# Optimization experiments

Hardware: AMD Instinct MI355X
Metric: run time of the kernel (lower is better)

Reference implementation:

```python
import jax, jax.numpy as jnp
import numpy as np

HID = 64      # hidden_dim
HEADS = 4     # attention heads
CH = HID // HEADS  # 16 per-head channels
EDIM = 6      # edge_dim
NEG = 0.2     # leaky_relu negative slope


def _glorot(key, shape):
    fan_in, fan_out = shape[0], shape[-1]
    s = np.sqrt(6.0 / (fan_in + fan_out)).astype(np.float32)
    return jax.random.uniform(key, shape, jnp.float32, -s, s)


def setup_inputs() -> dict:
    key = jax.random.key(0)
    ks = iter(jax.random.split(key, 48))
    N, E, T = 100000, 1200000, 20000
    inp = {
        "x": jax.random.normal(next(ks), (N, 7), jnp.float32),
        "pos": jax.random.normal(next(ks), (N, 3), jnp.float32),
        "node_type": jax.random.randint(next(ks), (N,), 0, 2),
        "edge_index": jax.random.randint(next(ks), (2, E), 0, N),
        "edge_attr": jax.random.normal(next(ks), (E, EDIM), jnp.float32),
        "num_tracks": T,
        "hidden_state": jax.random.normal(next(ks), (T, HID), jnp.float32),
        # params
        "type_emb": jax.random.normal(next(ks), (2, 8), jnp.float32),
        "enc_W1": _glorot(next(ks), (18, HID)), "enc_b1": jnp.zeros((HID,), jnp.float32),
        "enc_W2": _glorot(next(ks), (HID, HID)), "enc_b2": jnp.zeros((HID,), jnp.float32),
        "gru_Wi": _glorot(next(ks), (HID, 3 * HID)), "gru_bi": jnp.zeros((3 * HID,), jnp.float32),
        "gru_Wh": _glorot(next(ks), (HID, 3 * HID)), "gru_bh": jnp.zeros((3 * HID,), jnp.float32),
        "dec_W1": _glorot(next(ks), (HID, HID)), "dec_b1": jnp.zeros((HID,), jnp.float32),
        "dec_W2": _glorot(next(ks), (HID, 7)), "dec_b2": jnp.zeros((7,), jnp.float32),
    }
    for g in ("g1", "g2"):
        inp[g + "_Wl"] = _glorot(next(ks), (HID, HID))
        inp[g + "_bl"] = jnp.zeros((HID,), jnp.float32)
        inp[g + "_Wr"] = _glorot(next(ks), (HID, HID))
        inp[g + "_br"] = jnp.zeros((HID,), jnp.float32)
        inp[g + "_We"] = _glorot(next(ks), (EDIM, HID))
        inp[g + "_att"] = _glorot(next(ks), (HEADS, CH))
        inp[g + "_bias"] = jnp.zeros((HID,), jnp.float32)
    return inp


def _segment_softmax(e, seg, n):
    m = jax.ops.segment_max(e, seg, num_segments=n)
    m = jnp.where(jnp.isfinite(m), m, 0.0)
    ex = jnp.exp(e - m[seg])
    s = jax.ops.segment_sum(ex, seg, num_segments=n)
    return ex / (s[seg] + 1e-16)


def _gatv2(h, src, dst, eattr, Wl, bl, Wr, br, We, att, bias):
    N = h.shape[0]
    xl = (h @ Wl + bl).reshape(N, HEADS, CH)
    xr = (h @ Wr + br).reshape(N, HEADS, CH)
    ea = (eattr @ We).reshape(-1, HEADS, CH)
    g = jax.nn.leaky_relu(xl[src] + xr[dst] + ea, NEG)      # [E, H, C]
    e = jnp.einsum('ehc,hc->eh', g, att)                     # [E, H]
    alpha = _segment_softmax(e, dst, N)                      # [E, H]
    msg = xl[src] * alpha[..., None]                         # [E, H, C]
    out = jax.ops.segment_sum(msg, dst, num_segments=N)
    return out.reshape(N, HID) + bias, alpha


def reference(x, pos, node_type, edge_index, edge_attr, num_tracks, hidden_state,
              type_emb, enc_W1, enc_b1, enc_W2, enc_b2,
              g1_Wl, g1_bl, g1_Wr, g1_br, g1_We, g1_att, g1_bias,
              g2_Wl, g2_bl, g2_Wr, g2_br, g2_We, g2_att, g2_bias,
              gru_Wi, gru_bi, gru_Wh, gru_bh,
              dec_W1, dec_b1, dec_W2, dec_b2):
    N = x.shape[0]
    h = jnp.concatenate([x, pos, type_emb[node_type]], axis=-1)
    h = jax.nn.relu(h @ enc_W1 + enc_b1) @ enc_W2 + enc_b2

    # PyG GATv2Conv: add self loops, edge_attr fill_value='mean' (mean of incoming edges)
    src, dst = edge_index[0], edge_index[1]
    deg = jax.ops.segment_sum(jnp.ones(src.shape[0], jnp.float32), dst, num_segments=N)
    loop_attr = jax.ops.segment_sum(edge_attr, dst, num_segments=N) / jnp.maximum(deg, 1.0)[:, None]
    ar = jnp.arange(N)
    src_a = jnp.concatenate([src, ar])
    dst_a = jnp.concatenate([dst, ar])
    eattr_a = jnp.concatenate([edge_attr, loop_attr], axis=0)

    h1, a1 = _gatv2(h, src_a, dst_a, eattr_a, g1_Wl, g1_bl, g1_Wr, g1_br, g1_We, g1_att, g1_bias)
    h1 = jax.nn.relu(h1)
    h2, a2 = _gatv2(h1, src_a, dst_a, eattr_a, g2_Wl, g2_bl, g2_Wr, g2_br, g2_We, g2_att, g2_bias)

    # GRUCell on the first num_tracks nodes
    ht = h2[:num_tracks]
    gi = ht @ gru_Wi + gru_bi
    gh = hidden_state @ gru_Wh + gru_bh
    r = jax.nn.sigmoid(gi[:, :HID] + gh[:, :HID])
    z = jax.nn.sigmoid(gi[:, HID:2 * HID] + gh[:, HID:2 * HID])
    n = jnp.tanh(gi[:, 2 * HID:] + r * gh[:, 2 * HID:])
    new_tracks = (1.0 - z) * n + z * hidden_state

    new_full = jnp.concatenate([new_tracks, h2[num_tracks:]], axis=0)
    out = jax.nn.relu(new_full @ dec_W1 + dec_b1) @ dec_W2 + dec_b2  # [N, 7]
    final = out.at[:, :3].set(pos + out[:, :3])
    final = final.at[:, 3:6].set(x[:, :3] + out[:, 3:6])
    return final, new_full, a1, a2
```

## Files before the change

kernel.cpp:

```cpp
#include <hip/hip_runtime.h>

#define NEG 0.2f
#define LOG2E 1.44269504088896f
typedef unsigned short u16;

__device__ __forceinline__ float sigmoidf_(float v){ return 1.f/(1.f+__expf(-v)); }
__device__ __forceinline__ int rfl_(int v){ return __builtin_amdgcn_readfirstlane(v); }
__device__ __forceinline__ float bf2f_(unsigned u){ return __uint_as_float(u<<16); }
__device__ __forceinline__ u16 f2bf_(float f){
  unsigned u = __float_as_uint(f);
  u += 0x7FFFu + ((u>>16)&1u);
  return (u16)(u>>16);
}
template<int C>
__device__ __forceinline__ float dppadd_(float p){
  int r = __builtin_amdgcn_update_dpp(0, __float_as_int(p), C, 0xF, 0xF, true);
  return p + __int_as_float(r);
}
__device__ __forceinline__ float dppsum16_(float p){
  p = dppadd_<0x121>(p);
  p = dppadd_<0x122>(p);
  p = dppadd_<0x124>(p);
  p = dppadd_<0x128>(p);
  return p;
}

__device__ __forceinline__ void alpha_body_(int e, const int* __restrict__ ei,
    const float2* __restrict__ ms, float4* __restrict__ a, int E, int N)
{
  if (e >= E+N) return;
  int dst = (e<E)? ei[E+e] : (e-E);
  float4 r = a[e];
  const float2* mp = ms + (((unsigned)dst)<<2);
  float2 m0=mp[0], m1=mp[1], m2=mp[2], m3=mp[3];
  float4 o;
  o.x = exp2f(r.x - m0.x)*m0.y;
  o.y = exp2f(r.y - m1.x)*m1.y;
  o.z = exp2f(r.z - m2.x)*m2.y;
  o.w = exp2f(r.w - m3.x)*m3.y;
  a[e] = o;
}

__global__ __launch_bounds__(256) void encdeg_kernel(
    const float* __restrict__ x, const float* __restrict__ pos,
    const int* __restrict__ ntype, const float* __restrict__ temb,
    const float* __restrict__ W1, const float* __restrict__ b1,
    const float* __restrict__ W2, const float* __restrict__ b2,
    float* __restrict__ hout,
    const int* __restrict__ ei, int* __restrict__ deg,
    int encB, int E, int N)
{
  __shared__ float sW1[18*64];
  __shared__ float sW2[4096];
  __shared__ float fT[4][8*20];
  __shared__ float tT[4][8*64];
  if ((int)blockIdx.x >= encB){
    int e = ((int)blockIdx.x - encB)*256 + threadIdx.x;
    if (e < E) atomicAdd(deg + ei[E+e], 1);
    return;
  }
  for (int i=threadIdx.x; i<18*64; i+=256) sW1[i]=W1[i];
  for (int i=threadIdx.x; i<4096; i+=256)  sW2[i]=W2[i];
  __syncthreads();
  int lane = threadIdx.x & 63;
  int wid  = threadIdx.x >> 6;
  int n0 = (blockIdx.x*4 + wid)*8;
  if (n0 >= N) return;
  float b1v=b1[lane], b2v=b2[lane];
  #pragma unroll
  for (int m=0;m<8;m++){
    int n=n0+m; float fv=0.f;
    if (n<N){
      if (lane<7)       fv=x[(size_t)n*7+lane];
      else if (lane<10) fv=pos[(size_t)n*3+lane-7];
      else if (lane<18) fv=temb[ntype[n]*8+lane-10];
    }
    if (lane<20) fT[wid][m*20+lane]=fv;
  }
  float t[8];
  #pragma unroll
  for (int m=0;m<8;m++) t[m]=b1v;
  #pragma unroll 2
  for (int k=0;k<18;k++){
    float w=sW1[k*64+lane];
    #pragma unroll
    for (int m=0;m<8;m++) t[m] += fT[wid][m*20+k]*w;
  }
  #pragma unroll
  for (int m=0;m<8;m++){ t[m]=fmaxf(t[m],0.f); tT[wid][m*64+lane]=t[m]; }
  float o[8];
  #pragma unroll
  for (int m=0;m<8;m++) o[m]=b2v;
  #pragma unroll 2
  for (int k=0;k<64;k++){
    float w=sW2[k*64+lane];
    #pragma unroll
    for (int m=0;m<8;m++) o[m] += tT[wid][m*64+k]*w;
  }
  #pragma unroll
  for (int m=0;m<8;m++){ int n=n0+m; if (n<N) hout[(size_t)n*64+lane]=o[m]; }
}

__global__ __launch_bounds__(256) void alloc_kernel(
    const int* __restrict__ deg, int* __restrict__ offs, int* __restrict__ cursor,
    int* __restrict__ counter, int N)
{
  __shared__ int wsum[4], woff[4], sbase;
  int lane = threadIdx.x & 63, w = threadIdx.x >> 6;
  int base = blockIdx.x*1024 + threadIdx.x*4;
  int v[4]; int s=0;
  #pragma unroll
  for (int j=0;j<4;j++){ int i=base+j; v[j]=(i<N)?deg[i]:0; s+=v[j]; }
  int inc=s;
  #pragma unroll
  for (int d=1;d<64;d<<=1){ int t=__shfl_up(inc,d); if (lane>=d) inc+=t; }
  if (lane==63) wsum[w]=inc;
  __syncthreads();
  if (threadIdx.x==0){
    woff[0]=0; woff[1]=wsum[0]; woff[2]=wsum[0]+wsum[1]; woff[3]=wsum[0]+wsum[1]+wsum[2];
    sbase = atomicAdd(counter, woff[3]+wsum[3]);
  }
  __syncthreads();
  int excl = sbase + woff[w] + (inc - s);
  #pragma unroll
  for (int j=0;j<4;j++){
    int i=base+j;
    if (i<N){ offs[i]=excl; cursor[i]=excl; }
    excl+=v[j];
  }
}

__global__ __launch_bounds__(256) void xfrmfill_kernel(
    const float* __restrict__ hin,
    const float* __restrict__ Wl, const float* __restrict__ bl,
    const float* __restrict__ Wr, const float* __restrict__ br,
    u16* __restrict__ xlo, u16* __restrict__ xro,
    const int* __restrict__ ei, const float* __restrict__ eattr,
    int* __restrict__ cursor, float4* __restrict__ slots,
    int xfB, int E, int N)
{
  __shared__ float hT[4][16*64];
  if ((int)blockIdx.x >= xfB){
    int e = ((int)blockIdx.x - xfB)*256 + threadIdx.x;
    if (e < E){
      int dst = ei[E + e];
      unsigned slot = (unsigned)atomicAdd(cursor + dst, 1);
      const float2* ep = (const float2*)(eattr + (size_t)e*6);
      float2 p0=ep[0], p1=ep[1], p2=ep[2];
      float4 a, b;
      a.x = __int_as_float(e); a.y = __int_as_float(ei[e]);
      a.z = p0.x; a.w = p0.y;
      b.x = p1.x; b.y = p1.y; b.z = p2.x; b.w = p2.y;
      slots[slot*2u]   = a;
      slots[slot*2u+1] = b;
    }
    return;
  }
  int lane=threadIdx.x&63;
  int wid=threadIdx.x>>6;
  int n0=(blockIdx.x*4+wid)*16;
  if (n0>=N) return;
  #pragma unroll
  for (int m=0;m<16;m++){
    int n=n0+m;
    hT[wid][m*64+lane] = (n<N)? hin[(size_t)n*64+lane] : 0.f;
  }
  float blv=bl[lane], brv=br[lane];
  float al[16], ar[16];
  #pragma unroll
  for (int m=0;m<16;m++){ al[m]=blv; ar[m]=brv; }
  #pragma unroll 2
  for (int k=0;k<64;k++){
    float wl=Wl[k*64+lane], wr=Wr[k*64+lane];
    #pragma unroll
    for (int m=0;m<16;m++){
      float hb = hT[wid][m*64+k];
      al[m]+=hb*wl; ar[m]+=hb*wr;
    }
  }
  #pragma unroll
  for (int m=0;m<16;m++){
    int n=n0+m;
    if (n<N){ xlo[(((unsigned)n)<<6)+lane]=f2bf_(al[m]); xro[(((unsigned)n)<<6)+lane]=f2bf_(ar[m]); }
  }
}

__global__ __launch_bounds__(256) void xfrmalpha_kernel(
    const float* __restrict__ hin,
    const float* __restrict__ Wl, const float* __restrict__ bl,
    const float* __restrict__ Wr, const float* __restrict__ br,
    u16* __restrict__ xlo, u16* __restrict__ xro,
    const int* __restrict__ ei, const float2* __restrict__ ms1, float4* __restrict__ a1,
    int xfB, int E, int N)
{
  __shared__ float hT[4][16*64];
  if ((int)blockIdx.x >= xfB){
    int e = ((int)blockIdx.x - xfB)*256 + threadIdx.x;
    alpha_body_(e, ei, ms1, a1, E, N);
    return;
  }
  int lane=threadIdx.x&63;
  int wid=threadIdx.x>>6;
  int n0=(blockIdx.x*4+wid)*16;
  if (n0>=N) return;
  #pragma unroll
  for (int m=0;m<16;m++){
    int n=n0+m;
    hT[wid][m*64+lane] = (n<N)? hin[(size_t)n*64+lane] : 0.f;
  }
  float blv=bl[lane], brv=br[lane];
  float al[16], ar[16];
  #pragma unroll
  for (int m=0;m<16;m++){ al[m]=blv; ar[m]=brv; }
  #pragma unroll 2
  for (int k=0;k<64;k++){
    float wl=Wl[k*64+lane], wr=Wr[k*64+lane];
    #pragma unroll
    for (int m=0;m<16;m++){
      float hb = hT[wid][m*64+k];
      al[m]+=hb*wl; ar[m]+=hb*wr;
    }
  }
  #pragma unroll
  for (int m=0;m<16;m++){
    int n=n0+m;
    if (n<N){ xlo[(((unsigned)n)<<6)+lane]=f2bf_(al[m]); xro[(((unsigned)n)<<6)+lane]=f2bf_(ar[m]); }
  }
}

#define EDGE_STEP(EIDX, EADD, XV) do {                                       \
    float s_ = (XV) + xrv + (EADD);                                          \
    s_ = fmaxf(s_, NEG*s_);                                                  \
    float p_ = dppsum16_(s_*attv);                                           \
    if (isbase) aout[(((unsigned)(EIDX))<<2)+h] = p_;                        \
    if (__all(p_ <= mmax)) {                                                 \
      float w_ = exp2f(p_ - mmax);                                           \
      ssum += w_; acc += w_*(XV);                                            \
    } else {                                                                 \
      float mn_ = fmaxf(mmax, p_);                                           \
      float sc_ = exp2f(mmax - mn_);                                         \
      float w_  = exp2f(p_ - mn_);                                           \
      ssum = ssum*sc_ + w_;                                                  \
      acc  = acc*sc_ + w_*(XV);                                              \
      mmax = mn_;                                                            \
    }                                                                        \
  } while(0)

#define EDGE_PRE(J, OO) \
    float4 u##J = slots[(unsigned)(OO)*2u], v##J = slots[(unsigned)(OO)*2u+1u]; \
    int e##J = rfl_(__float_as_int(u##J.x)); \
    int s##J = rfl_(__float_as_int(u##J.y)); \
    unsigned xv##J = xlb[(((unsigned)s##J)<<6)+lane];

#define EDGE_BODY(J) \
    float d##J = u##J.z*we0 + u##J.w*we1 + v##J.x*we2 + v##J.y*we3 + v##J.z*we4 + v##J.w*we5; \
    dsum += d##J; \
    EDGE_STEP(e##J, d##J, bf2f_(xv##J));

__global__ __launch_bounds__(256) void gat_kernel(
    const float4* __restrict__ slots, const int* __restrict__ offs, const int* __restrict__ deg,
    const u16* __restrict__ xlb, const u16* __restrict__ xrb,
    const float* __restrict__ We, const float* __restrict__ att,
    const float* __restrict__ bias,
    float* __restrict__ aout, float2* __restrict__ msbuf,
    float* __restrict__ hout,
    int E, int N, int do_relu)
{
  int lane = threadIdx.x & 63;
  int n = blockIdx.x*4 + (threadIdx.x>>6);
  if (n >= N) return;
  float we0=We[lane], we1=We[64+lane], we2=We[128+lane],
        we3=We[192+lane], we4=We[256+lane], we5=We[320+lane];
  float attv = att[lane] * LOG2E;
  float bv = bias[lane];
  float xrv = bf2f_(xrb[(((unsigned)n)<<6)+lane]);
  int h = lane >> 4;
  bool isbase = (lane & 15) == 0;
  int o0 = rfl_(offs[n]);
  int dg = rfl_(deg[n]);
  int oend = o0 + dg;
  float mmax = -3.402823e38f, ssum=0.f, acc=0.f, dsum=0.f;
  int o = o0;
  for (; o+4 <= oend; o += 4){
    EDGE_PRE(0,o); EDGE_PRE(1,o+1); EDGE_PRE(2,o+2); EDGE_PRE(3,o+3);
    EDGE_BODY(0); EDGE_BODY(1); EDGE_BODY(2); EDGE_BODY(3);
  }
  for (; o < oend; ++o){
    EDGE_PRE(0,o);
    EDGE_BODY(0);
  }
  {
    float dS = dsum * (1.f/fmaxf((float)dg,1.f));
    float xvS = bf2f_((unsigned)xlb[(((unsigned)n)<<6)+lane]);
    EDGE_STEP(E+n, dS, xvS);
  }
  float sinv = 1.f/(ssum + 1e-16f);
  if (isbase) msbuf[(((unsigned)n)<<2)+h] = make_float2(mmax, sinv);
  float outv = acc*sinv + bv;
  if (do_relu) outv = fmaxf(outv, 0.f);
  hout[(((unsigned)n)<<6)+lane] = outv;
}

__global__ __launch_bounds__(256) void grudecalpha_kernel(
    const float* __restrict__ h2, const float* __restrict__ hid,
    const float* __restrict__ Wi, const float* __restrict__ bi,
    const float* __restrict__ Wh, const float* __restrict__ bh,
    const int* __restrict__ Tptr,
    const float* __restrict__ W1, const float* __restrict__ b1,
    const float* __restrict__ W2, const float* __restrict__ b2,
    const float* __restrict__ x, const float* __restrict__ pos,
    float* __restrict__ nf, float* __restrict__ fout,
    const int* __restrict__ ei,
    const float2* __restrict__ ms2, float4* __restrict__ a2,
    int gdB, int E, int N)
{
  __shared__ float sW2[448];
  __shared__ float sb2[8];
  __shared__ float tT[4][8*68];
  __shared__ float pT[4][8*68];
  if ((int)blockIdx.x >= gdB){
    int e = ((int)blockIdx.x - gdB)*256 + threadIdx.x;
    alpha_body_(e, ei, ms2, a2, E, N);
    return;
  }
  for (int i=threadIdx.x;i<448;i+=256) sW2[i]=W2[i];
  if (threadIdx.x<7)  sb2[threadIdx.x]=b2[threadIdx.x];
  __syncthreads();
  int lane = threadIdx.x & 63;
  int wid  = threadIdx.x >> 6;
  int n0 = (blockIdx.x*4 + wid)*8;
  if (n0 >= N) return;
  int T = *Tptr;
  float hv[8], nfv[8];
  #pragma unroll
  for (int m=0;m<8;m++){ int n=n0+m; hv[m] = (n<N)? h2[(size_t)n*64+lane] : 0.f; }
  if (n0 < T){
    float pv[8];
    #pragma unroll
    for (int m=0;m<8;m++){ int n=n0+m; pv[m] = (n<T)? hid[(size_t)n*64+lane] : 0.f; }
    #pragma unroll
    for (int m=0;m<8;m++){ tT[wid][m*68+lane]=hv[m]; pT[wid][m*68+lane]=pv[m]; }
    float gr[8],gz[8],gn[8],hr[8],hz[8],hn[8];
    #pragma unroll
    for (int m=0;m<8;m++){ gr[m]=0.f;gz[m]=0.f;gn[m]=0.f;hr[m]=0.f;hz[m]=0.f;hn[m]=0.f; }
    for (int k=0;k<64;k++){
      float wir=Wi[k*192+lane], wiz=Wi[k*192+64+lane], win=Wi[k*192+128+lane];
      float whr=Wh[k*192+lane], whz=Wh[k*192+64+lane], whn=Wh[k*192+128+lane];
      #pragma unroll
      for (int m=0;m<8;m++){
        float a=tT[wid][m*68+k], b=pT[wid][m*68+k];
        gr[m]+=a*wir; gz[m]+=a*wiz; gn[m]+=a*win;
        hr[m]+=b*whr; hz[m]+=b*whz; hn[m]+=b*whn;
      }
    }
    float bir=bi[lane], biz=bi[64+lane], bin=bi[128+lane];
    float bhr=bh[lane], bhz=bh[64+lane], bhn=bh[128+lane];
    #pragma unroll
    for (int m=0;m<8;m++){
      int n=n0+m;
      if (n<T){
        float r  = sigmoidf_(gr[m]+bir + hr[m]+bhr);
        float z  = sigmoidf_(gz[m]+biz + hz[m]+bhz);
        float nn = tanhf(gn[m]+bin + r*(hn[m]+bhn));
        nfv[m] = (1.f-z)*nn + z*pv[m];
      } else {
        nfv[m] = hv[m];
      }
    }
  } else {
    #pragma unroll
    for (int m=0;m<8;m++) nfv[m] = hv[m];
  }
  #pragma unroll
  for (int m=0;m<8;m++){ int n=n0+m; if (n<N) nf[(size_t)n*64+lane]=nfv[m]; }
  #pragma unroll
  for (int m=0;m<8;m++) tT[wid][m*68+lane]=nfv[m];
  float t[8];
  float b1v=b1[lane];
  #pragma unroll
  for (int m=0;m<8;m++) t[m]=b1v;
  #pragma unroll 2
  for (int k=0;k<64;k++){
    float w=W1[k*64+lane];
    #pragma unroll
    for (int m=0;m<8;m++) t[m] += tT[wid][m*68+k]*w;
  }
  #pragma unroll
  for (int m=0;m<8;m++) t[m]=fmaxf(t[m],0.f);
  #pragma unroll
  for (int m=0;m<8;m++) tT[wid][m*68+lane]=t[m];
  int mm = lane >> 3, cc = lane & 7;
  if (cc < 7){
    float a2v = sb2[cc];
    #pragma unroll 4
    for (int k=0;k<64;k++) a2v += tT[wid][mm*68+k]*sW2[k*7+cc];
    int n = n0+mm;
    if (n < N){
      if (cc<3)      a2v += pos[(size_t)n*3+cc];
      else if (cc<6) a2v += x[(size_t)n*7+(cc-3)];
      fout[(size_t)n*7+cc] = a2v;
    }
  }
}

extern "C" void kernel_launch(void* const* d_in, const int* in_sizes, int n_in,
                              void* d_out, int out_size, void* d_ws, size_t ws_size,
                              hipStream_t stream)
{
  const float* x     = (const float*)d_in[0];
  const float* pos   = (const float*)d_in[1];
  const int*   ntype = (const int*)d_in[2];
  const int*   eidx  = (const int*)d_in[3];
  const float* eattr = (const float*)d_in[4];
  const int*   Tptr  = (const int*)d_in[5];
  const float* hid   = (const float*)d_in[6];
  const float* temb  = (const float*)d_in[7];
  const float* encW1 = (const float*)d_in[8];
  const float* encb1 = (const float*)d_in[9];
  const float* encW2 = (const float*)d_in[10];
  const float* encb2 = (const float*)d_in[11];
  const float* gruWi = (const float*)d_in[12];
  const float* grubi = (const float*)d_in[13];
  const float* gruWh = (const float*)d_in[14];
  const float* grubh = (const float*)d_in[15];
  const float* decW1 = (const float*)d_in[16];
  const float* decb1 = (const float*)d_in[17];
  const float* decW2 = (const float*)d_in[18];
  const float* decb2 = (const float*)d_in[19];
  const float* gWl[2]  = {(const float*)d_in[20], (const float*)d_in[27]};
  const float* gbl[2]  = {(const float*)d_in[21], (const float*)d_in[28]};
  const float* gWr[2]  = {(const float*)d_in[22], (const float*)d_in[29]};
  const float* gbr[2]  = {(const float*)d_in[23], (const float*)d_in[30]};
  const float* gWe[2]  = {(const float*)d_in[24], (const float*)d_in[31]};
  const float* gatt[2] = {(const float*)d_in[25], (const float*)d_in[32]};
  const float* gbias[2]= {(const float*)d_in[26], (const float*)d_in[33]};

  int N  = in_sizes[0] / 7;
  int E  = in_sizes[3] / 2;
  int Ea = E + N;

  char* w = (char*)d_ws;
  float* A      = (float*)w; w += (size_t)N*64*sizeof(float);
  u16*   XL     = (u16*)w;  w += (size_t)N*64*sizeof(u16);
  u16*   XR     = (u16*)w;  w += (size_t)N*64*sizeof(u16);
  float2* msbuf1= (float2*)w; w += (size_t)N*4*sizeof(float2);
  float2* msbuf2= (float2*)w; w += (size_t)N*4*sizeof(float2);
  float4* slots = (float4*)w; w += (size_t)E*32;
  int*   deg    = (int*)w;   w += (size_t)N*sizeof(int);
  int*   counter= (int*)w;   w += 4*sizeof(int);
  int*   cursor = (int*)w;   w += (size_t)N*sizeof(int);
  int*   offs   = (int*)w;   w += (size_t)N*sizeof(int);

  float* out_final = (float*)d_out;
  float* out_nf    = out_final + (size_t)N*7;
  float* out_a1    = out_nf + (size_t)N*64;
  float* out_a2    = out_a1 + (size_t)Ea*4;

  hipMemsetAsync(deg, 0, ((size_t)N + 4)*sizeof(int), stream);

  int encB = (N+31)/32;
  int degB = (E+255)/256;
  encdeg_kernel<<<encB+degB, 256, 0, stream>>>(x,pos,ntype,temb,encW1,encb1,encW2,encb2,A,
      eidx, deg, encB, E, N);

  alloc_kernel<<<(N+1023)/1024, 256, 0, stream>>>(deg, offs, cursor, counter, N);

  int xfB = (N+63)/64;
  int flB = (E+255)/256;
  xfrmfill_kernel<<<xfB+flB, 256, 0, stream>>>(A, gWl[0], gbl[0], gWr[0], gbr[0], XL, XR,
      eidx, eattr, cursor, slots, xfB, E, N);

  gat_kernel<<<(N+3)/4, 256, 0, stream>>>(slots, offs, deg, XL, XR,
      gWe[0], gatt[0], gbias[0], out_a1, msbuf1, A, E, N, 1);

  int alB = (Ea+255)/256;
  xfrmalpha_kernel<<<xfB+alB, 256, 0, stream>>>(A, gWl[1], gbl[1], gWr[1], gbr[1], XL, XR,
      eidx, msbuf1, (float4*)out_a1, xfB, E, N);

  gat_kernel<<<(N+3)/4, 256, 0, stream>>>(slots, offs, deg, XL, XR,
      gWe[1], gatt[1], gbias[1], out_a2, msbuf2, A, E, N, 0);

  int gdB = (N+31)/32;
  grudecalpha_kernel<<<gdB+alB, 256, 0, stream>>>(A, hid, gruWi, grubi, gruWh, grubh, Tptr,
      decW1, decb1, decW2, decb2, x, pos, out_nf, out_final,
      eidx, msbuf2, (float4*)out_a2, gdB, E, N);
}
```

Before: 499.1 us.

## Interleave alpha normalization blocks into GAT and GRU kernels, stage weights in LDS

Moves the layer-1 alpha normalization out of the transform kernel and into the layer-2 GAT kernel, with its blocks spread evenly among the GAT blocks. The GRU/decoder kernel likewise spreads its compute blocks evenly among the alpha blocks. The intent is to overlap memory-bound alpha writes with latency-bound gather work and to balance block types across CUs. The standalone transform kernel now stages Wl/Wr in shared memory, which raises LDS use to about 48KB per block and may lower occupancy.

```diff
diff --git a/kernel.cpp b/kernel.cpp
--- a/kernel.cpp
+++ b/kernel.cpp
@@ -185,20 +185,16 @@
   }
 }
 
-__global__ __launch_bounds__(256) void xfrmalpha_kernel(
+__global__ __launch_bounds__(256) void xfrm_kernel(
     const float* __restrict__ hin,
     const float* __restrict__ Wl, const float* __restrict__ bl,
     const float* __restrict__ Wr, const float* __restrict__ br,
-    u16* __restrict__ xlo, u16* __restrict__ xro,
-    const int* __restrict__ ei, const float2* __restrict__ ms1, float4* __restrict__ a1,
-    int xfB, int E, int N)
-{
+    u16* __restrict__ xlo, u16* __restrict__ xro, int N)
+{
+  __shared__ float sWl[4096], sWr[4096];
   __shared__ float hT[4][16*64];
-  if ((int)blockIdx.x >= xfB){
-    int e = ((int)blockIdx.x - xfB)*256 + threadIdx.x;
-    alpha_body_(e, ei, ms1, a1, E, N);
-    return;
-  }
+  for (int i=threadIdx.x;i<4096;i+=256){ sWl[i]=Wl[i]; sWr[i]=Wr[i]; }
+  __syncthreads();
   int lane=threadIdx.x&63;
   int wid=threadIdx.x>>6;
   int n0=(blockIdx.x*4+wid)*16;
@@ -214,7 +210,7 @@
   for (int m=0;m<16;m++){ al[m]=blv; ar[m]=brv; }
   #pragma unroll 2
   for (int k=0;k<64;k++){
-    float wl=Wl[k*64+lane], wr=Wr[k*64+lane];
+    float wl=sWl[k*64+lane], wr=sWr[k*64+lane];
     #pragma unroll
     for (int m=0;m<16;m++){
       float hb = hT[wid][m*64+k];
@@ -257,17 +253,15 @@
     dsum += d##J; \
     EDGE_STEP(e##J, d##J, bf2f_(xv##J));
 
-__global__ __launch_bounds__(256) void gat_kernel(
+__device__ __forceinline__ void gat_node_(int n,
     const float4* __restrict__ slots, const int* __restrict__ offs, const int* __restrict__ deg,
     const u16* __restrict__ xlb, const u16* __restrict__ xrb,
     const float* __restrict__ We, const float* __restrict__ att,
     const float* __restrict__ bias,
     float* __restrict__ aout, float2* __restrict__ msbuf,
-    float* __restrict__ hout,
-    int E, int N, int do_relu)
+    float* __restrict__ hout, int E, int N, int do_relu)
 {
   int lane = threadIdx.x & 63;
-  int n = blockIdx.x*4 + (threadIdx.x>>6);
   if (n >= N) return;
   float we0=We[lane], we1=We[64+lane], we2=We[128+lane],
         we3=We[192+lane], we4=We[256+lane], we5=We[320+lane];
@@ -301,6 +295,41 @@
   hout[(((unsigned)n)<<6)+lane] = outv;
 }
 
+__global__ __launch_bounds__(256) void gat_kernel(
+    const float4* __restrict__ slots, const int* __restrict__ offs, const int* __restrict__ deg,
+    const u16* __restrict__ xlb, const u16* __restrict__ xrb,
+    const float* __restrict__ We, const float* __restrict__ att,
+    const float* __restrict__ bias,
+    float* __restrict__ aout, float2* __restrict__ msbuf,
+    float* __restrict__ hout,
+    int E, int N, int do_relu)
+{
+  int n = blockIdx.x*4 + (threadIdx.x>>6);
+  gat_node_(n, slots, offs, deg, xlb, xrb, We, att, bias, aout, msbuf, hout, E, N, do_relu);
+}
+
+__global__ __launch_bounds__(256) void gatalpha_kernel(
+    const float4* __restrict__ slots, const int* __restrict__ offs, const int* __restrict__ deg,
+    const u16* __restrict__ xlb, const u16* __restrict__ xrb,
+    const float* __restrict__ We, const float* __restrict__ att,
+    const float* __restrict__ bias,
+    float* __restrict__ aout, float2* __restrict__ msbuf,
+    float* __restrict__ hout,
+    const int* __restrict__ ei, const float2* __restrict__ ms1, float4* __restrict__ a1,
+    int S, int alB, int E, int N, int do_relu)
+{
+  int idx = blockIdx.x;
+  int q = idx / S;
+  if (idx % S == 0 && q < alB){
+    alpha_body_(q*256 + (int)threadIdx.x, ei, ms1, a1, E, N);
+    return;
+  }
+  int nA = min(q + 1, alB);
+  int gid = idx - nA;
+  int n = gid*4 + (threadIdx.x>>6);
+  gat_node_(n, slots, offs, deg, xlb, xrb, We, att, bias, aout, msbuf, hout, E, N, do_relu);
+}
+
 __global__ __launch_bounds__(256) void grudecalpha_kernel(
     const float* __restrict__ h2, const float* __restrict__ hid,
     const float* __restrict__ Wi, const float* __restrict__ bi,
@@ -312,15 +341,20 @@
     float* __restrict__ nf, float* __restrict__ fout,
     const int* __restrict__ ei,
     const float2* __restrict__ ms2, float4* __restrict__ a2,
-    int gdB, int E, int N)
+    int S, int gdB, int E, int N)
 {
   __shared__ float sW2[448];
   __shared__ float sb2[8];
   __shared__ float tT[4][8*68];
   __shared__ float pT[4][8*68];
-  if ((int)blockIdx.x >= gdB){
-    int e = ((int)blockIdx.x - gdB)*256 + threadIdx.x;
-    alpha_body_(e, ei, ms2, a2, E, N);
+  int idx = blockIdx.x;
+  int q = idx / S;
+  int gblk;
+  if (idx % S == 0 && q < gdB){
+    gblk = q;
+  } else {
+    int nG = min(q + 1, gdB);
+    alpha_body_((idx - nG)*256 + (int)threadIdx.x, ei, ms2, a2, E, N);
     return;
   }
   for (int i=threadIdx.x;i<448;i+=256) sW2[i]=W2[i];
@@ -328,7 +362,7 @@
   __syncthreads();
   int lane = threadIdx.x & 63;
   int wid  = threadIdx.x >> 6;
-  int n0 = (blockIdx.x*4 + wid)*8;
+  int n0 = (gblk*4 + wid)*8;
   if (n0 >= N) return;
   int T = *Tptr;
   float hv[8], nfv[8];
@@ -470,18 +504,21 @@
   xfrmfill_kernel<<<xfB+flB, 256, 0, stream>>>(A, gWl[0], gbl[0], gWr[0], gbr[0], XL, XR,
       eidx, eattr, cursor, slots, xfB, E, N);
 
-  gat_kernel<<<(N+3)/4, 256, 0, stream>>>(slots, offs, deg, XL, XR,
+  int gatB = (N+3)/4;
+  gat_kernel<<<gatB, 256, 0, stream>>>(slots, offs, deg, XL, XR,
       gWe[0], gatt[0], gbias[0], out_a1, msbuf1, A, E, N, 1);
 
+  xfrm_kernel<<<xfB, 256, 0, stream>>>(A, gWl[1], gbl[1], gWr[1], gbr[1], XL, XR, N);
+
   int alB = (Ea+255)/256;
-  xfrmalpha_kernel<<<xfB+alB, 256, 0, stream>>>(A, gWl[1], gbl[1], gWr[1], gbr[1], XL, XR,
-      eidx, msbuf1, (float4*)out_a1, xfB, E, N);
-
-  gat_kernel<<<(N+3)/4, 256, 0, stream>>>(slots, offs, deg, XL, XR,
-      gWe[1], gatt[1], gbias[1], out_a2, msbuf2, A, E, N, 0);
+  int Sg = (gatB + alB) / alB;
+  gatalpha_kernel<<<gatB+alB, 256, 0, stream>>>(slots, offs, deg, XL, XR,
+      gWe[1], gatt[1], gbias[1], out_a2, msbuf2, A,
+      eidx, msbuf1, (float4*)out_a1, Sg, alB, E, N, 0);
 
   int gdB = (N+31)/32;
+  int Sd = (gdB + alB) / gdB;
   grudecalpha_kernel<<<gdB+alB, 256, 0, stream>>>(A, hid, gruWi, grubi, gruWh, grubh, Tptr,
       decW1, decb1, decW2, decb2, x, pos, out_nf, out_final,
-      eidx, msbuf2, (float4*)out_a2, gdB, E, N);
-}
+      eidx, msbuf2, (float4*)out_a2, Sd, gdB, E, N);
+}
```

Measured after the change: 540.5 us. 1.08x slower.
